# Kernel tuning notes

Measured on AMD Instinct MI355X. Metric: run time of the kernel, lower is better.

Reference implementation:

```python
import math
import jax, jax.numpy as jnp
import numpy as np

SINKHORN_ITERS = 5
SINKHORN_REG = 1.0
D_MODEL, KDIM, VDIM = 512, 512, 512
B, T, N = 8, 2048, 2048


def _xavier(key, shape):
    fan_in, fan_out = shape[0], shape[1]
    bound = math.sqrt(6.0 / (fan_in + fan_out))
    return jax.random.uniform(key, shape, jnp.float32, -bound, bound)


def setup_inputs() -> dict:
    key = jax.random.key(0)
    kq, kk, kv, kQ, kK, kV = jax.random.split(key, 6)
    return {
        "q": jax.random.normal(kq, (T, D_MODEL), jnp.float32),
        "k": jax.random.normal(kk, (B, N, KDIM), jnp.float32),
        "v": jax.random.normal(kv, (B, N, VDIM), jnp.float32),
        "Q": _xavier(kQ, (D_MODEL, D_MODEL)),
        "K": _xavier(kK, (KDIM, D_MODEL)),
        "V": _xavier(kV, (VDIM, D_MODEL)),
    }


def _cdist(q, k):
    # q: [T, d], k: [B, N, d] -> Euclidean distances [B, T, N]
    q2 = jnp.sum(q * q, axis=-1)            # [T]
    k2 = jnp.sum(k * k, axis=-1)            # [B, N]
    qk = jnp.einsum('td,bnd->btn', q, k)    # [B, T, N]
    sq = q2[None, :, None] + k2[:, None, :] - 2.0 * qk
    return jnp.sqrt(jnp.maximum(sq, 0.0))


def _sinkhorn(q, k, iters, reg):
    costs = _cdist(q, k)                    # [B, T, N]
    Kmat = -costs / reg
    num_params = k.shape[1]
    num_tokens = q.shape[0]
    log_a = -jnp.log(jnp.float32(num_params))
    log_b = jnp.float32(0.0)
    u = jnp.zeros((k.shape[0], 1, num_params), Kmat.dtype)
    v = jnp.zeros((k.shape[0], num_tokens, 1), Kmat.dtype)
    for _ in range(iters):
        u = log_a - jax.scipy.special.logsumexp(Kmat + v, axis=1, keepdims=True)
        v = log_b - jax.scipy.special.logsumexp(Kmat + u, axis=2, keepdims=True)
    return jnp.exp(Kmat + u + v)


def reference(q, k, v, Q, K, V):
    qp = q @ Q                               # [T, d_model]
    kp = k @ K                               # [B, N, d_model]
    vp = v @ V                               # [B, N, d_model]
    pi = _sinkhorn(qp, kp, SINKHORN_ITERS, SINKHORN_REG)  # [B, T, N]
    return jnp.einsum('btn,bnd->btd', pi, vp)              # [B, T, d_model]
```

## Files before the change

### kernel.cpp

```cpp
#include <hip/hip_runtime.h>
#include <math.h>

#define TT 2048
#define NP 2048
#define BB 8
#define DD 512
#define TCH 8

#define LOG_A (-7.6246189861593985f)
#define CC 30.0f
#define E30 1.0686475e13f

typedef __attribute__((ext_vector_type(8))) _Float16 f16x8;
typedef __attribute__((ext_vector_type(4))) _Float16 f16x4;
typedef __attribute__((ext_vector_type(4))) float f32x4;

#define MFMA_F16(a, b, c)  __builtin_amdgcn_mfma_f32_16x16x32_f16((a), (b), (c), 0, 0, 0)

__device__ __forceinline__ float f16u2f(unsigned short u) {
    union { unsigned short s; _Float16 h; } v; v.s = u;
    return (float)v.h;
}

__device__ __forceinline__ void gload16(const void* g, void* l) {
    __builtin_amdgcn_global_load_lds(
        (const __attribute__((address_space(1))) void*)g,
        (__attribute__((address_space(3))) void*)l, 16, 0, 0);
}

__device__ __forceinline__ void frag_step_f16(
    const _Float16* sA, const _Float16* sB,
    int lane, int wm, int wn, f32x4 acc[4][4])
{
    const int sb = (lane >> 4) << 11;
    const int rl = (lane & 15) << 4;
    f16x8 a[4], b[4];
    #pragma unroll
    for (int i = 0; i < 4; ++i) {
        a[i] = *(const f16x8*)((const char*)sA + sb + ((wm + i * 16) << 4) + rl);
        b[i] = *(const f16x8*)((const char*)sB + sb + ((wn + i * 16) << 4) + rl);
    }
    #pragma unroll
    for (int i = 0; i < 4; ++i)
        #pragma unroll
        for (int j = 0; j < 4; ++j)
            acc[i][j] = MFMA_F16(a[i], b[j], acc[i][j]);
}

__device__ __forceinline__ void zero_acc(f32x4 acc[4][4]) {
    #pragma unroll
    for (int i = 0; i < 4; ++i)
        #pragma unroll
        for (int j = 0; j < 4; ++j)
            acc[i][j] = (f32x4){0.f, 0.f, 0.f, 0.f};
}

__device__ __forceinline__ void store_plain(
    float* C, int N, int row0, int col0, int lane, int wm, int wn, f32x4 acc[4][4])
{
    #pragma unroll
    for (int i = 0; i < 4; ++i)
        #pragma unroll
        for (int j = 0; j < 4; ++j) {
            int colg = col0 + wn + j * 16 + (lane & 15);
            int rowb = row0 + wm + i * 16 + ((lane >> 4) << 2);
            #pragma unroll
            for (int r = 0; r < 4; ++r)
                C[(size_t)(rowb + r) * N + colg] = acc[i][j][r];
        }
}

__global__ __launch_bounds__(256) void transpose_f16(
    const float* __restrict__ X, _Float16* __restrict__ oT, int R, int C)
{
    const size_t zoff = (size_t)blockIdx.z * R * C;
    const float* Xb = X + zoff;
    _Float16* ob = oT + zoff;
    __shared__ float t[64][65];
    const int bx = blockIdx.x * 64;
    const int by = blockIdx.y * 64;
    const int tx = threadIdx.x & 63, ty = threadIdx.x >> 6;
    #pragma unroll
    for (int r = ty; r < 64; r += 4)
        t[r][tx] = Xb[(size_t)(by + r) * C + bx + tx];
    __syncthreads();
    #pragma unroll
    for (int r = ty; r < 64; r += 4)
        ob[(size_t)(bx + r) * R + by + tx] = (_Float16)t[tx][r];
}

template<int OUT>
__global__ __launch_bounds__(256) void gemm_proj_f16(
    const float* __restrict__ A, const _Float16* __restrict__ Bt,
    _Float16* __restrict__ C, int M, int N, int K)
{
    __shared__ __attribute__((aligned(16))) _Float16 sA[4096], sB[4096];
    const int tid = threadIdx.x;
    const int lane = tid & 63;
    const int row0 = blockIdx.y * 128;
    const int col0 = blockIdx.x * 128;
    const int wm = ((tid >> 7) & 1) * 64;
    const int wn = ((tid >> 6) & 1) * 64;
    f32x4 acc[4][4];
    zero_acc(acc);

    for (int k0 = 0; k0 < K; k0 += 32) {
        __syncthreads();
        #pragma unroll
        for (int q = 0; q < 2; ++q) {
            int o = (tid + (q << 8)) << 4;
            int s = o >> 11;
            int r = (o & 2047) >> 4;
            gload16(Bt + (size_t)(col0 + r) * K + k0 + s * 8, (char*)sB + o);
            const float* src = A + (size_t)(row0 + r) * K + k0 + s * 8;
            float4 f0 = *(const float4*)src;
            float4 f1 = *(const float4*)(src + 4);
            _Float16 hs[8] = {(_Float16)f0.x, (_Float16)f0.y,
                              (_Float16)f0.z, (_Float16)f0.w,
                              (_Float16)f1.x, (_Float16)f1.y,
                              (_Float16)f1.z, (_Float16)f1.w};
            *(f16x8*)((char*)sA + o) = *(f16x8*)hs;
        }
        __syncthreads();
        frag_step_f16(sA, sB, lane, wm, wn, acc);
    }
    #pragma unroll
    for (int i = 0; i < 4; ++i)
        #pragma unroll
        for (int j = 0; j < 4; ++j) {
            int colg = col0 + wn + j * 16 + (lane & 15);
            int rowb = row0 + wm + i * 16 + ((lane >> 4) << 2);
            if (OUT == 1) {
                #pragma unroll
                for (int r = 0; r < 4; ++r)
                    C[(size_t)(rowb + r) * N + colg] = (_Float16)acc[i][j][r];
            } else {
                int b = rowb >> 11;
                int n0 = rowb & (NP - 1);
                _Float16 h4[4];
                #pragma unroll
                for (int r = 0; r < 4; ++r) h4[r] = (_Float16)acc[i][j][r];
                *(f16x4*)(C + (size_t)b * DD * NP + (size_t)colg * NP + n0) =
                    *(f16x4*)h4;
            }
        }
}

__global__ __launch_bounds__(256) void rownorm_f16(
    const _Float16* __restrict__ X, float* __restrict__ o, int rows)
{
    int w = blockIdx.x * 4 + (threadIdx.x >> 6);
    int lane = threadIdx.x & 63;
    if (w >= rows) return;
    f16x8 v = *(const f16x8*)(X + (size_t)w * DD + lane * 8);
    float s = 0.f;
    #pragma unroll
    for (int j = 0; j < 8; ++j) {
        float x = (float)v[j];
        s = fmaf(x, x, s);
    }
    #pragma unroll
    for (int off = 32; off; off >>= 1) s += __shfl_down(s, off, 64);
    if (lane == 0) o[w] = s;
}

__global__ __launch_bounds__(256) void gemm_cost_f16(
    const _Float16* __restrict__ A, const _Float16* __restrict__ B,
    const float* __restrict__ q2, const float* __restrict__ k2,
    _Float16* __restrict__ E)
{
    const int bid = blockIdx.x;
    const int sid = ((bid & 7) << 8) | (bid >> 3);
    const int b  = sid >> 8;
    const int by = (sid >> 4) & 15;
    const int bx = sid & 15;

    const _Float16* Bb = B + (size_t)b * NP * DD;
    const float* k2b = k2 + (size_t)b * NP;
    _Float16* Cb = E + (size_t)b * TT * NP;

    __shared__ __attribute__((aligned(16))) _Float16 sA[2][4096], sB[2][4096];
    const int tid = threadIdx.x;
    const int lane = tid & 63;
    const int row0 = by * 128;
    const int col0 = bx * 128;
    const int wm = ((tid >> 7) & 1) * 64;
    const int wn = ((tid >> 6) & 1) * 64;
    f32x4 acc[4][4];
    zero_acc(acc);

    auto STAGE = [&](int buf, int k0) {
        #pragma unroll
        for (int q = 0; q < 2; ++q) {
            int o = (tid + (q << 8)) << 4;
            int s = o >> 11;
            int r = (o & 2047) >> 4;
            gload16(A + (size_t)(row0 + r) * DD + k0 + s * 8, (char*)&sA[buf][0] + o);
            gload16(Bb + (size_t)(col0 + r) * DD + k0 + s * 8, (char*)&sB[buf][0] + o);
        }
    };

    STAGE(0, 0);
    __syncthreads();
    int cur = 0;
    for (int k0 = 0; k0 < DD; k0 += 32) {
        if (k0 + 32 < DD) STAGE(cur ^ 1, k0 + 32);
        frag_step_f16(&sA[cur][0], &sB[cur][0], lane, wm, wn, acc);
        __syncthreads();
        cur ^= 1;
    }
    #pragma unroll
    for (int i = 0; i < 4; ++i)
        #pragma unroll
        for (int j = 0; j < 4; ++j) {
            int colg = col0 + wn + j * 16 + (lane & 15);
            float k2v = k2b[colg];
            int rowb = row0 + wm + i * 16 + ((lane >> 4) << 2);
            #pragma unroll
            for (int r = 0; r < 4; ++r) {
                float sq = q2[rowb + r] + k2v - 2.f * acc[i][j][r];
                float dist = sqrtf(fmaxf(sq, 0.f));
                float e = fminf(__expf(CC - dist), 60000.f);
                Cb[(size_t)(rowb + r) * NP + colg] = (_Float16)e;
            }
        }
}

__global__ __launch_bounds__(256) void init_ones(float* __restrict__ Y)
{
    Y[blockIdx.x * 256 + threadIdx.x] = 1.0f;
}

__global__ __launch_bounds__(256) void u_part(
    const _Float16* __restrict__ E, const float* __restrict__ Y,
    float* __restrict__ ps)
{
    const int b = blockIdx.z;
    const int tch = blockIdx.y;
    const int lane = threadIdx.x & 63;
    const int p = threadIdx.x >> 6;
    const int n0 = blockIdx.x * 128;
    const unsigned* Eb = (const unsigned*)(E + (size_t)b * TT * NP + n0);
    const float* Yb = Y + (size_t)b * TT;

    float s0 = 0.f, s1 = 0.f;
    const int t0 = tch * (TT / TCH) + p * (TT / TCH / 4);
    for (int tt = 0; tt < TT / TCH / 4; ++tt) {
        int t = t0 + tt;
        unsigned w = Eb[(size_t)t * (NP / 2) + lane];
        float yv = Yb[t];
        s0 = fmaf(f16u2f((unsigned short)(w & 0xFFFFu)), yv, s0);
        s1 = fmaf(f16u2f((unsigned short)(w >> 16)),     yv, s1);
    }
    __shared__ float sss[4][128];
    sss[p][2 * lane] = s0; sss[p][2 * lane + 1] = s1;
    __syncthreads();
    if (p == 0) {
        s0 += sss[1][2 * lane]     + sss[2][2 * lane]     + sss[3][2 * lane];
        s1 += sss[1][2 * lane + 1] + sss[2][2 * lane + 1] + sss[3][2 * lane + 1];
        size_t o = ((size_t)b * TCH + tch) * NP + n0 + 2 * lane;
        ps[o] = s0; ps[o + 1] = s1;
    }
}

__global__ __launch_bounds__(256) void u_combine(
    const float* __restrict__ ps, float* __restrict__ U)
{
    int gid = blockIdx.x * 256 + threadIdx.x;
    int b = gid >> 11;
    int n = gid & (NP - 1);
    float S = 0.f;
    #pragma unroll
    for (int c = 0; c < TCH; ++c)
        S += ps[((size_t)b * TCH + c) * NP + n];
    U[gid] = __expf(LOG_A + CC - __logf(S));
}

template<bool WP>
__global__ __launch_bounds__(256) void v_update_q(
    const _Float16* __restrict__ E, const float* __restrict__ U,
    float* __restrict__ Y, _Float16* __restrict__ P)
{
    const int b = blockIdx.y;
    const int t = blockIdx.x;
    const uint4* Eb = (const uint4*)(E + ((size_t)b * TT + t) * NP);
    const float* Ub = U + (size_t)b * NP;
    const int tid = threadIdx.x;

    uint4 w = Eb[tid];
    const int n0 = tid * 8;
    float4 u0 = *(const float4*)(Ub + n0);
    float4 u1 = *(const float4*)(Ub + n0 + 4);
    float ev[8];
    ev[0] = f16u2f((unsigned short)(w.x & 0xFFFFu));
    ev[1] = f16u2f((unsigned short)(w.x >> 16));
    ev[2] = f16u2f((unsigned short)(w.y & 0xFFFFu));
    ev[3] = f16u2f((unsigned short)(w.y >> 16));
    ev[4] = f16u2f((unsigned short)(w.z & 0xFFFFu));
    ev[5] = f16u2f((unsigned short)(w.z >> 16));
    ev[6] = f16u2f((unsigned short)(w.w & 0xFFFFu));
    ev[7] = f16u2f((unsigned short)(w.w >> 16));
    float uv[8] = {u0.x, u0.y, u0.z, u0.w, u1.x, u1.y, u1.z, u1.w};

    float s = 0.f;
    #pragma unroll
    for (int j = 0; j < 8; ++j) s = fmaf(ev[j], uv[j], s);

    #pragma unroll
    for (int off = 32; off; off >>= 1) s += __shfl_down(s, off, 64);

    __shared__ float sw[4];
    __shared__ float Sall;
    if ((tid & 63) == 0) sw[tid >> 6] = s;
    __syncthreads();
    if (tid == 0) {
        float S = sw[0] + sw[1] + sw[2] + sw[3];
        Y[(size_t)b * TT + t] = E30 / S;
        Sall = S;
    }
    if (WP) {
        __syncthreads();
        float invS = 1.0f / Sall;
        _Float16 hp[8];
        #pragma unroll
        for (int j = 0; j < 8; ++j)
            hp[j] = (_Float16)(ev[j] * uv[j] * invS);
        *(f16x8*)(P + ((size_t)b * TT + t) * NP + n0) = *(f16x8*)hp;
    }
}

__global__ __launch_bounds__(256) void gemm_pi_f16(
    const _Float16* __restrict__ P, const _Float16* __restrict__ B,
    float* __restrict__ out)
{
    const int bid = blockIdx.x;
    const int sid = ((bid & 7) << 6) | (bid >> 3);
    const int b  = sid >> 6;
    const int by = (sid >> 2) & 15;
    const int bx = sid & 3;

    const _Float16* Pb = P + (size_t)b * TT * NP;
    const _Float16* Bb = B + (size_t)b * DD * NP;
    float* Cb = out + (size_t)b * TT * DD;

    __shared__ __attribute__((aligned(16))) _Float16 sA[2][4096], sB[2][4096];
    const int tid = threadIdx.x;
    const int lane = tid & 63;
    const int row0 = by * 128;
    const int col0 = bx * 128;
    const int wm = ((tid >> 7) & 1) * 64;
    const int wn = ((tid >> 6) & 1) * 64;
    f32x4 acc[4][4];
    zero_acc(acc);

    auto STAGE = [&](int buf, int k0) {
        #pragma unroll
        for (int q = 0; q < 2; ++q) {
            int o = (tid + (q << 8)) << 4;
            int s = o >> 11;
            int r = (o & 2047) >> 4;
            gload16(Pb + (size_t)(row0 + r) * NP + k0 + s * 8, (char*)&sA[buf][0] + o);
            gload16(Bb + (size_t)(col0 + r) * NP + k0 + s * 8, (char*)&sB[buf][0] + o);
        }
    };

    STAGE(0, 0);
    __syncthreads();
    int cur = 0;
    for (int k0 = 0; k0 < NP; k0 += 32) {
        if (k0 + 32 < NP) STAGE(cur ^ 1, k0 + 32);
        frag_step_f16(&sA[cur][0], &sB[cur][0], lane, wm, wn, acc);
        __syncthreads();
        cur ^= 1;
    }
    store_plain(Cb, DD, row0, col0, lane, wm, wn, acc);
}

extern "C" void kernel_launch(void* const* d_in, const int* in_sizes, int n_in,
                              void* d_out, int out_size, void* d_ws, size_t ws_size,
                              hipStream_t stream)
{
    const float* q  = (const float*)d_in[0];
    const float* k  = (const float*)d_in[1];
    const float* v  = (const float*)d_in[2];
    const float* Qw = (const float*)d_in[3];
    const float* Kw = (const float*)d_in[4];
    const float* Vw = (const float*)d_in[5];
    float* out = (float*)d_out;

    char* base = (char*)d_ws;
    _Float16* E16 = (_Float16*)base;
    char* p2 = base + (size_t)BB * TT * NP * 2;
    _Float16* P   = (_Float16*)p2; p2 += (size_t)BB * TT * NP * 2;
    _Float16* qpf = (_Float16*)p2; p2 += (size_t)TT * DD * 2;
    _Float16* kpf = (_Float16*)p2; p2 += (size_t)BB * NP * DD * 2;
    _Float16* vpt = (_Float16*)p2; p2 += (size_t)BB * DD * NP * 2;
    float* q2 = (float*)p2; p2 += (size_t)TT * 4;
    float* k2 = (float*)p2; p2 += (size_t)BB * NP * 4;
    float* U  = (float*)p2; p2 += (size_t)BB * NP * 4;
    float* Y  = (float*)p2; p2 += (size_t)BB * TT * 4;
    float* ps = (float*)p2; p2 += (size_t)BB * TCH * NP * 4;

    _Float16* wq = (_Float16*)base;
    _Float16* wk = wq + 262144;
    _Float16* wv = wk + 262144;

    dim3 blk(256);

    transpose_f16<<<dim3(8, 8, 1), blk, 0, stream>>>(Qw, wq, 512, 512);
    transpose_f16<<<dim3(8, 8, 1), blk, 0, stream>>>(Kw, wk, 512, 512);
    transpose_f16<<<dim3(8, 8, 1), blk, 0, stream>>>(Vw, wv, 512, 512);

    gemm_proj_f16<1><<<dim3(4, 16, 1), blk, 0, stream>>>(q, wq, qpf, TT, DD, DD);
    gemm_proj_f16<1><<<dim3(4, 128, 1), blk, 0, stream>>>(k, wk, kpf, BB * NP, DD, DD);
    gemm_proj_f16<2><<<dim3(4, 128, 1), blk, 0, stream>>>(v, wv, vpt, BB * NP, DD, DD);

    rownorm_f16<<<dim3(TT / 4), blk, 0, stream>>>(qpf, q2, TT);
    rownorm_f16<<<dim3((BB * NP) / 4), blk, 0, stream>>>(kpf, k2, BB * NP);

    gemm_cost_f16<<<dim3(2048), blk, 0, stream>>>(qpf, kpf, q2, k2, E16);

    init_ones<<<dim3(BB * TT / 256), blk, 0, stream>>>(Y);
    for (int it = 0; it < 5; ++it) {
        u_part<<<dim3(NP / 128, TCH, BB), blk, 0, stream>>>(E16, Y, ps);
        u_combine<<<dim3(BB * NP / 256), blk, 0, stream>>>(ps, U);
        if (it < 4)
            v_update_q<false><<<dim3(TT, BB), blk, 0, stream>>>(E16, U, Y, nullptr);
        else
            v_update_q<true><<<dim3(TT, BB), blk, 0, stream>>>(E16, U, Y, P);
    }

    gemm_pi_f16<<<dim3(512), blk, 0, stream>>>(P, vpt, out);
}
```

Baseline: 425.7 us.

## Fuse Sinkhorn row and column updates into one pass and stage cost-tile stores

Each Sinkhorn iteration used to read E twice, once in a column-sum kernel and once in a row-update kernel. The new kernel reads a 32-row tile of E once, computes the row normalizers in place with a shared-memory reduction, and accumulates the weighted column partial sums in the same pass. That removes one full pass over the 64 MB E matrix per iteration and also drops the init_ones kernel. The cost GEMM epilogue now writes its tile through LDS so global stores become coalesced 16-byte rows, and u_combine uses a division in place of exp and log. The price is three block barriers per 8-row group, more registers held across the loop, and a 64-way partial-sum buffer that u_combine has to reduce.

```diff
diff --git a/kernel.cpp b/kernel.cpp
--- a/kernel.cpp
+++ b/kernel.cpp
@@ -5,11 +5,11 @@
 #define NP 2048
 #define BB 8
 #define DD 512
-#define TCH 8
 
 #define LOG_A (-7.6246189861593985f)
 #define CC 30.0f
 #define E30 1.0686475e13f
+#define K0U 5.2180055e9f
 
 typedef __attribute__((ext_vector_type(8))) _Float16 f16x8;
 typedef __attribute__((ext_vector_type(4))) _Float16 f16x4;
@@ -209,58 +209,134 @@
         __syncthreads();
         cur ^= 1;
     }
+
+    _Float16* half0 = &sA[0][0];
+    _Float16* half1 = &sB[0][0];
     #pragma unroll
     for (int i = 0; i < 4; ++i)
         #pragma unroll
         for (int j = 0; j < 4; ++j) {
-            int colg = col0 + wn + j * 16 + (lane & 15);
-            float k2v = k2b[colg];
-            int rowb = row0 + wm + i * 16 + ((lane >> 4) << 2);
+            int lc = wn + j * 16 + (lane & 15);
+            float k2v = k2b[col0 + lc];
+            int lrb = wm + i * 16 + ((lane >> 4) << 2);
             #pragma unroll
             for (int r = 0; r < 4; ++r) {
-                float sq = q2[rowb + r] + k2v - 2.f * acc[i][j][r];
+                float sq = q2[row0 + lrb + r] + k2v - 2.f * acc[i][j][r];
                 float dist = sqrtf(fmaxf(sq, 0.f));
                 float e = fminf(__expf(CC - dist), 60000.f);
-                Cb[(size_t)(rowb + r) * NP + colg] = (_Float16)e;
-            }
-        }
-}
-
-__global__ __launch_bounds__(256) void init_ones(float* __restrict__ Y)
-{
-    Y[blockIdx.x * 256 + threadIdx.x] = 1.0f;
-}
-
-__global__ __launch_bounds__(256) void u_part(
-    const _Float16* __restrict__ E, const float* __restrict__ Y,
+                if (wm == 0) half0[(lrb + r) * 128 + lc] = (_Float16)e;
+                else         half1[(lrb + r - 64) * 128 + lc] = (_Float16)e;
+            }
+        }
+    __syncthreads();
+    {
+        const int lr16 = tid >> 4;
+        const int c8 = (tid & 15) * 8;
+        #pragma unroll
+        for (int m = 0; m < 4; ++m) {
+            int lr = m * 16 + lr16;
+            f16x8 vrow = *(const f16x8*)(half0 + lr * 128 + c8);
+            *(f16x8*)(Cb + (size_t)(row0 + lr) * NP + col0 + c8) = vrow;
+        }
+        #pragma unroll
+        for (int m = 0; m < 4; ++m) {
+            int lr = 64 + m * 16 + lr16;
+            f16x8 vrow = *(const f16x8*)(half1 + (lr - 64) * 128 + c8);
+            *(f16x8*)(Cb + (size_t)(row0 + lr) * NP + col0 + c8) = vrow;
+        }
+    }
+}
+
+template<bool FIRST>
+__global__ __launch_bounds__(256) void sink_fused(
+    const _Float16* __restrict__ E, const float* __restrict__ U,
     float* __restrict__ ps)
 {
-    const int b = blockIdx.z;
-    const int tch = blockIdx.y;
-    const int lane = threadIdx.x & 63;
-    const int p = threadIdx.x >> 6;
-    const int n0 = blockIdx.x * 128;
-    const unsigned* Eb = (const unsigned*)(E + (size_t)b * TT * NP + n0);
-    const float* Yb = Y + (size_t)b * TT;
-
-    float s0 = 0.f, s1 = 0.f;
-    const int t0 = tch * (TT / TCH) + p * (TT / TCH / 4);
-    for (int tt = 0; tt < TT / TCH / 4; ++tt) {
-        int t = t0 + tt;
-        unsigned w = Eb[(size_t)t * (NP / 2) + lane];
-        float yv = Yb[t];
-        s0 = fmaf(f16u2f((unsigned short)(w & 0xFFFFu)), yv, s0);
-        s1 = fmaf(f16u2f((unsigned short)(w >> 16)),     yv, s1);
-    }
-    __shared__ float sss[4][128];
-    sss[p][2 * lane] = s0; sss[p][2 * lane + 1] = s1;
-    __syncthreads();
-    if (p == 0) {
-        s0 += sss[1][2 * lane]     + sss[2][2 * lane]     + sss[3][2 * lane];
-        s1 += sss[1][2 * lane + 1] + sss[2][2 * lane + 1] + sss[3][2 * lane + 1];
-        size_t o = ((size_t)b * TCH + tch) * NP + n0 + 2 * lane;
-        ps[o] = s0; ps[o + 1] = s1;
-    }
+    const int b = blockIdx.y;
+    const int t0 = blockIdx.x * 32;
+    const int tid = threadIdx.x;
+    const int n0 = tid * 8;
+    const _Float16* Eb = E + ((size_t)b * TT + t0) * NP;
+
+    float u8[8];
+    if (!FIRST) {
+        float4 a = *(const float4*)(U + (size_t)b * NP + n0);
+        float4 c = *(const float4*)(U + (size_t)b * NP + n0 + 4);
+        u8[0] = a.x; u8[1] = a.y; u8[2] = a.z; u8[3] = a.w;
+        u8[4] = c.x; u8[5] = c.y; u8[6] = c.z; u8[7] = c.w;
+    }
+
+    float cs[8] = {0.f, 0.f, 0.f, 0.f, 0.f, 0.f, 0.f, 0.f};
+    __shared__ float red[8][256];
+    __shared__ float yy[8];
+
+    #pragma unroll
+    for (int g = 0; g < 4; ++g) {
+        uint4 ev[8];
+        #pragma unroll
+        for (int r = 0; r < 8; ++r)
+            ev[r] = *(const uint4*)(Eb + (size_t)(g * 8 + r) * NP + n0);
+
+        if (!FIRST) {
+            #pragma unroll
+            for (int r = 0; r < 8; ++r) {
+                float d = 0.f;
+                d = fmaf(f16u2f((unsigned short)(ev[r].x & 0xFFFFu)), u8[0], d);
+                d = fmaf(f16u2f((unsigned short)(ev[r].x >> 16)),     u8[1], d);
+                d = fmaf(f16u2f((unsigned short)(ev[r].y & 0xFFFFu)), u8[2], d);
+                d = fmaf(f16u2f((unsigned short)(ev[r].y >> 16)),     u8[3], d);
+                d = fmaf(f16u2f((unsigned short)(ev[r].z & 0xFFFFu)), u8[4], d);
+                d = fmaf(f16u2f((unsigned short)(ev[r].z >> 16)),     u8[5], d);
+                d = fmaf(f16u2f((unsigned short)(ev[r].w & 0xFFFFu)), u8[6], d);
+                d = fmaf(f16u2f((unsigned short)(ev[r].w >> 16)),     u8[7], d);
+                red[r][tid] = d;
+            }
+            __syncthreads();
+            {
+                int w = tid >> 6, lane = tid & 63;
+                #pragma unroll
+                for (int rr = 0; rr < 2; ++rr) {
+                    int r = w * 2 + rr;
+                    float s = red[r][lane] + red[r][lane + 64] +
+                              red[r][lane + 128] + red[r][lane + 192];
+                    #pragma unroll
+                    for (int off = 32; off; off >>= 1)
+                        s += __shfl_down(s, off, 64);
+                    if (lane == 0) yy[r] = E30 / s;
+                }
+            }
+            __syncthreads();
+            #pragma unroll
+            for (int r = 0; r < 8; ++r) {
+                float yv = yy[r];
+                cs[0] = fmaf(f16u2f((unsigned short)(ev[r].x & 0xFFFFu)), yv, cs[0]);
+                cs[1] = fmaf(f16u2f((unsigned short)(ev[r].x >> 16)),     yv, cs[1]);
+                cs[2] = fmaf(f16u2f((unsigned short)(ev[r].y & 0xFFFFu)), yv, cs[2]);
+                cs[3] = fmaf(f16u2f((unsigned short)(ev[r].y >> 16)),     yv, cs[3]);
+                cs[4] = fmaf(f16u2f((unsigned short)(ev[r].z & 0xFFFFu)), yv, cs[4]);
+                cs[5] = fmaf(f16u2f((unsigned short)(ev[r].z >> 16)),     yv, cs[5]);
+                cs[6] = fmaf(f16u2f((unsigned short)(ev[r].w & 0xFFFFu)), yv, cs[6]);
+                cs[7] = fmaf(f16u2f((unsigned short)(ev[r].w >> 16)),     yv, cs[7]);
+            }
+            __syncthreads();
+        } else {
+            #pragma unroll
+            for (int r = 0; r < 8; ++r) {
+                cs[0] += f16u2f((unsigned short)(ev[r].x & 0xFFFFu));
+                cs[1] += f16u2f((unsigned short)(ev[r].x >> 16));
+                cs[2] += f16u2f((unsigned short)(ev[r].y & 0xFFFFu));
+                cs[3] += f16u2f((unsigned short)(ev[r].y >> 16));
+                cs[4] += f16u2f((unsigned short)(ev[r].z & 0xFFFFu));
+                cs[5] += f16u2f((unsigned short)(ev[r].z >> 16));
+                cs[6] += f16u2f((unsigned short)(ev[r].w & 0xFFFFu));
+                cs[7] += f16u2f((unsigned short)(ev[r].w >> 16));
+            }
+        }
+    }
+
+    size_t o = ((size_t)b * 64 + blockIdx.x) * NP + n0;
+    *(float4*)(ps + o)     = make_float4(cs[0], cs[1], cs[2], cs[3]);
+    *(float4*)(ps + o + 4) = make_float4(cs[4], cs[5], cs[6], cs[7]);
 }
 
 __global__ __launch_bounds__(256) void u_combine(
@@ -270,16 +346,15 @@
     int b = gid >> 11;
     int n = gid & (NP - 1);
     float S = 0.f;
-    #pragma unroll
-    for (int c = 0; c < TCH; ++c)
-        S += ps[((size_t)b * TCH + c) * NP + n];
-    U[gid] = __expf(LOG_A + CC - __logf(S));
-}
-
-template<bool WP>
-__global__ __launch_bounds__(256) void v_update_q(
+    #pragma unroll 8
+    for (int c = 0; c < 64; ++c)
+        S += ps[((size_t)b * 64 + c) * NP + n];
+    U[gid] = K0U / S;
+}
+
+__global__ __launch_bounds__(256) void v_final(
     const _Float16* __restrict__ E, const float* __restrict__ U,
-    float* __restrict__ Y, _Float16* __restrict__ P)
+    _Float16* __restrict__ P)
 {
     const int b = blockIdx.y;
     const int t = blockIdx.x;
@@ -305,7 +380,6 @@
     float s = 0.f;
     #pragma unroll
     for (int j = 0; j < 8; ++j) s = fmaf(ev[j], uv[j], s);
-
     #pragma unroll
     for (int off = 32; off; off >>= 1) s += __shfl_down(s, off, 64);
 
@@ -313,20 +387,14 @@
     __shared__ float Sall;
     if ((tid & 63) == 0) sw[tid >> 6] = s;
     __syncthreads();
-    if (tid == 0) {
-        float S = sw[0] + sw[1] + sw[2] + sw[3];
-        Y[(size_t)b * TT + t] = E30 / S;
-        Sall = S;
-    }
-    if (WP) {
-        __syncthreads();
-        float invS = 1.0f / Sall;
-        _Float16 hp[8];
-        #pragma unroll
-        for (int j = 0; j < 8; ++j)
-            hp[j] = (_Float16)(ev[j] * uv[j] * invS);
-        *(f16x8*)(P + ((size_t)b * TT + t) * NP + n0) = *(f16x8*)hp;
-    }
+    if (tid == 0) Sall = sw[0] + sw[1] + sw[2] + sw[3];
+    __syncthreads();
+    float invS = 1.0f / Sall;
+    _Float16 hp[8];
+    #pragma unroll
+    for (int j = 0; j < 8; ++j)
+        hp[j] = (_Float16)(ev[j] * uv[j] * invS);
+    *(f16x8*)(P + ((size_t)b * TT + t) * NP + n0) = *(f16x8*)hp;
 }
 
 __global__ __launch_bounds__(256) void gemm_pi_f16(
@@ -398,8 +466,7 @@
     float* q2 = (float*)p2; p2 += (size_t)TT * 4;
     float* k2 = (float*)p2; p2 += (size_t)BB * NP * 4;
     float* U  = (float*)p2; p2 += (size_t)BB * NP * 4;
-    float* Y  = (float*)p2; p2 += (size_t)BB * TT * 4;
-    float* ps = (float*)p2; p2 += (size_t)BB * TCH * NP * 4;
+    float* ps = (float*)p2; p2 += (size_t)BB * 64 * NP * 4;
 
     _Float16* wq = (_Float16*)base;
     _Float16* wk = wq + 262144;
@@ -420,15 +487,13 @@
 
     gemm_cost_f16<<<dim3(2048), blk, 0, stream>>>(qpf, kpf, q2, k2, E16);
 
-    init_ones<<<dim3(BB * TT / 256), blk, 0, stream>>>(Y);
-    for (int it = 0; it < 5; ++it) {
-        u_part<<<dim3(NP / 128, TCH, BB), blk, 0, stream>>>(E16, Y, ps);
+    sink_fused<true><<<dim3(TT / 32, BB), blk, 0, stream>>>(E16, U, ps);
+    u_combine<<<dim3(BB * NP / 256), blk, 0, stream>>>(ps, U);
+    for (int it = 0; it < 4; ++it) {
+        sink_fused<false><<<dim3(TT / 32, BB), blk, 0, stream>>>(E16, U, ps);
         u_combine<<<dim3(BB * NP / 256), blk, 0, stream>>>(ps, U);
-        if (it < 4)
-            v_update_q<false><<<dim3(TT, BB), blk, 0, stream>>>(E16, U, Y, nullptr);
-        else
-            v_update_q<true><<<dim3(TT, BB), blk, 0, stream>>>(E16, U, Y, P);
-    }
+    }
+    v_final<<<dim3(TT, BB), blk, 0, stream>>>(E16, U, P);
 
     gemm_pi_f16<<<dim3(512), blk, 0, stream>>>(P, vpt, out);
 }
```

Result: no change. 424.1 us (-0.4%).
